# Performance work log

Hardware: AMD Instinct MI355X
Metric: run time of the kernel (lower is better)

The kernel has to match this reference:

```python
import jax, jax.numpy as jnp
import numpy as np

NUM_HEADS = 16


def dct_matrix(n, dtype=jnp.float32):
    # Orthonormal DCT-II matrix, matching the torch double-loop construction.
    i = jnp.arange(n, dtype=dtype)[:, None]
    j = jnp.arange(n, dtype=dtype)[None, :]
    m = jnp.sqrt(2.0 / n) * jnp.cos(jnp.pi * i * (2.0 * j + 1.0) / (2.0 * n))
    m = m.at[0, :].set(jnp.sqrt(1.0 / n))
    return m


def setup_inputs() -> dict:
    key = jax.random.key(0)
    ks = jax.random.split(key, 7)
    B, N, C = 8, 1024, 1024
    n_tasks, n_frq = 10, 3000
    return {
        "x": jax.random.normal(ks[0], (B, N, C), jnp.float32),
        "W_qkv": jax.random.normal(ks[1], (3 * C, C), jnp.float32) * 0.02,
        "W_proj": jax.random.normal(ks[2], (C, C), jnp.float32) * 0.02,
        "b_proj": jnp.zeros((C,), jnp.float32),
        "coef_k": jax.random.normal(ks[3], (n_tasks, n_frq), jnp.float32),
        "coef_v": jax.random.normal(ks[4], (n_tasks, n_frq), jnp.float32),
        "indices": jax.random.randint(ks[5], (n_tasks, n_frq), 0, C * C, jnp.int32),
        "task": 4,
    }


def _dct_lora_weight(coef, idx, Bm, d, dtype):
    # Scatter per-task frequency coefficients into the d x d DCT plane and sum
    # across tasks (sum commutes with the linear inverse transform), then
    # inverse 2D DCT: W = Bm^T @ S @ Bm.
    S = jnp.zeros((d * d,), dtype).at[idx.reshape(-1)].add(coef.reshape(-1))
    return Bm.T @ S.reshape(d, d) @ Bm


def reference(x, W_qkv, W_proj, b_proj, coef_k, coef_v, indices, task):
    B, N, C = x.shape
    H = NUM_HEADS
    hd = C // H
    scale = hd ** (-0.5)

    qkv = (x @ W_qkv.T).reshape(B, N, 3, H, hd).transpose(2, 0, 3, 1, 4)
    q, k, v = qkv[0], qkv[1], qkv[2]  # each (B, H, N, hd)

    T = task + 1  # tasks 0..task participate
    Bm = dct_matrix(C, x.dtype)
    Wk = _dct_lora_weight(coef_k[:T], indices[:T], Bm, C, x.dtype)
    Wv = _dct_lora_weight(coef_v[:T], indices[:T], Bm, C, x.dtype)

    # F.linear(x, W) == x @ W.T ; reshape to heads as in torch code
    k = k + (x @ Wk.T).reshape(B, N, H, hd).transpose(0, 2, 1, 3)
    v = v + (x @ Wv.T).reshape(B, N, H, hd).transpose(0, 2, 1, 3)

    attn = jax.nn.softmax(jnp.einsum("bhnd,bhmd->bhnm", q, k) * scale, axis=-1)
    out = jnp.einsum("bhnm,bhmd->bhnd", attn, v)
    out = out.transpose(0, 2, 1, 3).reshape(B, N, C)
    return out @ W_proj.T + b_proj
```

## Files before the change

kernel.cpp:

```cpp
#include <hip/hip_runtime.h>
#include <math.h>

#define NFRQ 3000

typedef __bf16 bf16;
typedef __attribute__((ext_vector_type(8))) __bf16 bf16x8;
typedef __attribute__((ext_vector_type(4))) __bf16 bf16x4;
typedef __attribute__((ext_vector_type(4))) float floatx4;

__device__ __forceinline__ floatx4 mfma16(bf16x8 a, bf16x8 b, floatx4 c) {
  return __builtin_amdgcn_mfma_f32_16x16x32_bf16(a, b, c, 0, 0, 0);
}

__device__ __forceinline__ void async_load16(const bf16* g, bf16* l) {
  __builtin_amdgcn_global_load_lds(
      (const __attribute__((address_space(1))) unsigned int*)g,
      (__attribute__((address_space(3))) unsigned int*)l, 16, 0, 0);
}

__device__ __forceinline__ float fexp2(float x) {
  return __builtin_amdgcn_exp2f(x);
}

__global__ __launch_bounds__(256) void prep_kernel(
    const float* __restrict__ W_qkv, const float* __restrict__ W_proj,
    const float* __restrict__ x, const float* __restrict__ Sf,
    bf16* __restrict__ Bmtb, bf16* __restrict__ Wcbq,
    bf16* __restrict__ Wprojb, bf16* __restrict__ xb,
    bf16* __restrict__ S2b) {
  int r = blockIdx.x;
  if (r < 1024) {
    int base = r * 1024 + (int)threadIdx.x * 4;
    const float cst = 0.04419417382415922f;
    const float w = 1.5339807878856412e-3f;
    bf16x4 o;
#pragma unroll
    for (int u = 0; u < 4; ++u) {
      int t = base + u;
      int j = t >> 10, i = t & 1023;
      int K = (i * (2 * j + 1)) & 4095;
      float v = (i == 0) ? 0.03125f : cst * __cosf((float)K * w);
      o[u] = (__bf16)v;
    }
    *(bf16x4*)&Bmtb[base] = o;
    return;
  }
  const float* src;
  bf16* dst;
  float scale = 1.0f;
  int i;
  if (r < 2048) {
    i = (r - 1024) * 256 + threadIdx.x;
    src = W_qkv; dst = Wcbq;
    scale = 0.18033688011112042f;
  } else if (r < 3072) {
    i = (r - 2048) * 256 + threadIdx.x;
    src = W_proj; dst = Wprojb;
  } else if (r < 11264) {
    i = (r - 3072) * 256 + threadIdx.x;
    src = x; dst = xb;
  } else {
    i = (r - 11264) * 256 + threadIdx.x;
    src = Sf; dst = S2b;
  }
  float4 f = ((const float4*)src)[i];
  bf16x4 o = {(__bf16)(f.x * scale), (__bf16)(f.y * scale),
              (__bf16)(f.z * scale), (__bf16)(f.w * scale)};
  *(bf16x4*)&dst[(size_t)i * 4] = o;
}

__global__ __launch_bounds__(256) void scatter_s(const float* __restrict__ coef_k,
                                                 const float* __restrict__ coef_v,
                                                 const int* __restrict__ idx,
                                                 const int* __restrict__ task,
                                                 float* __restrict__ S) {
  int nz = blockIdx.x * 256 + threadIdx.x;
  if (nz >= 10 * NFRQ || nz >= (*task + 1) * NFRQ) return;
  int id = idx[nz];
  atomicAdd(S + id, coef_k[nz]);
  atomicAdd(S + (1u << 20) + id, coef_v[nz]);
}

__global__ __launch_bounds__(512, 2) void gemm256_qkv(const bf16* __restrict__ A,
                                                      const bf16* __restrict__ B,
                                                      bf16* __restrict__ Cb,
                                                      bf16* __restrict__ vt) {
  __shared__ bf16 As[2][256][64];
  __shared__ bf16 Bs[2][256][64];
  int t = threadIdx.x, w = t >> 6, lane = t & 63;
  int q15 = lane & 15, quad = lane >> 4;
  int lid = blockIdx.x + gridDim.x * blockIdx.y;
  int band = gridDim.y >> 3;
  int xcd = lid & 7, tt = lid >> 3;
  int by = xcd * band + tt % band;
  int bx = tt / band;
  int m0 = by * 256, n0 = bx * 256;
  int wm = (w >> 2) * 128, wn = (w & 3) * 64;

  floatx4 acc[8][4];
#pragma unroll
  for (int i = 0; i < 8; ++i)
#pragma unroll
    for (int j = 0; j < 4; ++j) acc[i][j] = (floatx4){0.f, 0.f, 0.f, 0.f};

  int sr = lane >> 3, sc = lane & 7;
  const bf16* Agl = A + (size_t)(m0 + sr) * 1024 + (sc ^ sr) * 8;
  const bf16* Bgl = B + (size_t)(n0 + sr) * 1024 + (sc ^ sr) * 8;

#pragma unroll
  for (int s = 0; s < 4; ++s) {
    int rb = w * 32 + s * 8;
    async_load16(Agl + (size_t)rb * 1024, &As[0][rb][0]);
    async_load16(Bgl + (size_t)rb * 1024, &Bs[0][rb][0]);
  }

  for (int kt = 0; kt < 16; ++kt) {
    int cur = kt & 1;
    if (kt + 1 < 16) {
      int k0 = (kt + 1) * 64;
#pragma unroll
      for (int s = 0; s < 4; ++s) {
        int rb = w * 32 + s * 8;
        async_load16(Agl + (size_t)rb * 1024 + k0, &As[cur ^ 1][rb][0]);
        async_load16(Bgl + (size_t)rb * 1024 + k0, &Bs[cur ^ 1][rb][0]);
      }
      asm volatile("s_waitcnt vmcnt(8)\n\ts_barrier" ::: "memory");
    } else {
      asm volatile("s_waitcnt vmcnt(0)\n\ts_barrier" ::: "memory");
    }
    int rp = q15 & 7;
#pragma unroll
    for (int kk = 0; kk < 2; ++kk) {
      int kc = kk * 4 + quad;
      int ksw = (kc ^ rp) * 8;
      bf16x8 af[8], bfr[4];
#pragma unroll
      for (int i = 0; i < 8; ++i)
        af[i] = *(const bf16x8*)&As[cur][wm + i * 16 + q15][ksw];
#pragma unroll
      for (int j = 0; j < 4; ++j)
        bfr[j] = *(const bf16x8*)&Bs[cur][wn + j * 16 + q15][ksw];
#pragma unroll
      for (int i = 0; i < 8; ++i)
#pragma unroll
        for (int j = 0; j < 4; ++j)
          acc[i][j] = mfma16(af[i], bfr[j], acc[i][j]);
    }
    asm volatile("s_waitcnt lgkmcnt(0)\n\ts_barrier" ::: "memory");
  }

  if (n0 >= 2048) {
#pragma unroll
    for (int i = 0; i < 8; ++i) {
      int gm = m0 + wm + i * 16 + quad * 4;
      int p = gm >> 10, mi = gm & 1023;
#pragma unroll
      for (int j = 0; j < 4; ++j) {
        int vchan = (n0 + wn - 2048) + j * 16 + q15;
        bf16x4 pk = {(__bf16)acc[i][j][0], (__bf16)acc[i][j][1],
                     (__bf16)acc[i][j][2], (__bf16)acc[i][j][3]};
        *(bf16x4*)&vt[((((size_t)p << 10) | vchan) << 10) | mi] = pk;
      }
    }
    return;
  }

#pragma unroll
  for (int i = 0; i < 8; ++i)
#pragma unroll
    for (int r = 0; r < 4; ++r) {
      int gm = m0 + wm + i * 16 + quad * 4 + r;
      size_t rowo = (size_t)gm * 3072 + n0 + wn;
#pragma unroll
      for (int j = 0; j < 4; ++j) {
        int col = j * 16 + q15;
        Cb[rowo + col] = (__bf16)acc[i][j][r];
      }
    }
}

__global__ __launch_bounds__(512) void gemm256_proj(const bf16* __restrict__ A,
                                                    const bf16* __restrict__ B,
                                                    float* __restrict__ Cf,
                                                    const float* __restrict__ bias) {
  __shared__ bf16 As[2][256][64];
  __shared__ bf16 Bs[2][128][64];
  int t = threadIdx.x, w = t >> 6, lane = t & 63;
  int q15 = lane & 15, quad = lane >> 4;
  int lid = blockIdx.x + gridDim.x * blockIdx.y;
  int band = gridDim.y >> 3;
  int xcd = lid & 7, tt = lid >> 3;
  int by = xcd * band + tt % band;
  int bx = tt / band;
  int m0 = by * 256, n0 = bx * 128;
  int wm = (w >> 2) * 128, wn = (w & 3) * 32;

  floatx4 acc[8][2];
#pragma unroll
  for (int i = 0; i < 8; ++i)
#pragma unroll
    for (int j = 0; j < 2; ++j) acc[i][j] = (floatx4){0.f, 0.f, 0.f, 0.f};

  int sr = lane >> 3, sc = lane & 7;
  const bf16* Agl = A + (size_t)(m0 + sr) * 1024 + (sc ^ sr) * 8;
  const bf16* Bgl = B + (size_t)(n0 + sr) * 1024 + (sc ^ sr) * 8;

#pragma unroll
  for (int s = 0; s < 4; ++s)
    async_load16(Agl + (size_t)(w * 32 + s * 8) * 1024, &As[0][w * 32 + s * 8][0]);
#pragma unroll
  for (int s = 0; s < 2; ++s)
    async_load16(Bgl + (size_t)(w * 16 + s * 8) * 1024, &Bs[0][w * 16 + s * 8][0]);

  for (int kt = 0; kt < 16; ++kt) {
    int cur = kt & 1;
    if (kt + 1 < 16) {
      int k0 = (kt + 1) * 64;
#pragma unroll
      for (int s = 0; s < 4; ++s)
        async_load16(Agl + (size_t)(w * 32 + s * 8) * 1024 + k0,
                     &As[cur ^ 1][w * 32 + s * 8][0]);
#pragma unroll
      for (int s = 0; s < 2; ++s)
        async_load16(Bgl + (size_t)(w * 16 + s * 8) * 1024 + k0,
                     &Bs[cur ^ 1][w * 16 + s * 8][0]);
      asm volatile("s_waitcnt vmcnt(6)\n\ts_barrier" ::: "memory");
    } else {
      asm volatile("s_waitcnt vmcnt(0)\n\ts_barrier" ::: "memory");
    }
    int rp = q15 & 7;
#pragma unroll
    for (int kk = 0; kk < 2; ++kk) {
      int kc = kk * 4 + quad;
      int ksw = (kc ^ rp) * 8;
      bf16x8 af[8], bfr[2];
#pragma unroll
      for (int i = 0; i < 8; ++i)
        af[i] = *(const bf16x8*)&As[cur][wm + i * 16 + q15][ksw];
#pragma unroll
      for (int j = 0; j < 2; ++j)
        bfr[j] = *(const bf16x8*)&Bs[cur][wn + j * 16 + q15][ksw];
#pragma unroll
      for (int i = 0; i < 8; ++i)
#pragma unroll
        for (int j = 0; j < 2; ++j)
          acc[i][j] = mfma16(af[i], bfr[j], acc[i][j]);
    }
    asm volatile("s_waitcnt lgkmcnt(0)\n\ts_barrier" ::: "memory");
  }

#pragma unroll
  for (int i = 0; i < 8; ++i)
#pragma unroll
    for (int r = 0; r < 4; ++r) {
      int gm = m0 + wm + i * 16 + quad * 4 + r;
      size_t rowo = (size_t)gm * 1024 + n0 + wn;
#pragma unroll
      for (int j = 0; j < 2; ++j) {
        int col = j * 16 + q15;
        Cf[rowo + col] = acc[i][j][r] + bias[n0 + wn + col];
      }
    }
}

__global__ __launch_bounds__(256) void gemm64_bf16_nt(const bf16* __restrict__ A,
                                                      const bf16* __restrict__ B,
                                                      bf16* __restrict__ Cb,
                                                      float* __restrict__ Cf,
                                                      const float* __restrict__ addend,
                                                      const float* __restrict__ bias,
                                                      bf16* __restrict__ vt,
                                                      int vt_col0,
                                                      int N) {
  __shared__ bf16 As[2][4][64][8];
  __shared__ bf16 Bs[2][4][64][8];
  size_t zoff = (size_t)blockIdx.z << 20;
  B += zoff;
  if (Cb) Cb += zoff;
  if (addend) addend += zoff;
  int t = threadIdx.x, w = t >> 6, lane = t & 63;
  int q15 = lane & 15, quad = lane >> 4;
  int lid = blockIdx.x + gridDim.x * blockIdx.y;
  int band = gridDim.y >> 3;
  int xcd = lid & 7, tt = lid >> 3;
  int by = xcd * band + tt % band;
  int bx = tt / band;
  int m0 = by * 64, n0 = bx * 64;
  int wm = (w >> 1) * 32, wn = (w & 1) * 32;
  floatx4 acc[2][2];
#pragma unroll
  for (int i = 0; i < 2; ++i)
#pragma unroll
    for (int j = 0; j < 2; ++j) acc[i][j] = (floatx4){0.f, 0.f, 0.f, 0.f};

  const bf16* Ag = A + (size_t)(m0 + lane) * 1024 + w * 8;
  const bf16* Bg = B + (size_t)(n0 + lane) * 1024 + w * 8;

  async_load16(Ag, &As[0][w][0][0]);
  async_load16(Bg, &Bs[0][w][0][0]);

  for (int it = 0; it < 32; ++it) {
    int cur = it & 1;
    __syncthreads();
    if (it + 1 < 32) {
      int k0 = (it + 1) * 32;
      async_load16(Ag + k0, &As[cur ^ 1][w][0][0]);
      async_load16(Bg + k0, &Bs[cur ^ 1][w][0][0]);
    }
    bf16x8 af[2], bfr[2];
#pragma unroll
    for (int i = 0; i < 2; ++i)
      af[i] = *(const bf16x8*)&As[cur][quad][wm + i * 16 + q15][0];
#pragma unroll
    for (int j = 0; j < 2; ++j)
      bfr[j] = *(const bf16x8*)&Bs[cur][quad][wn + j * 16 + q15][0];
#pragma unroll
    for (int i = 0; i < 2; ++i)
#pragma unroll
      for (int j = 0; j < 2; ++j) acc[i][j] = mfma16(af[i], bfr[j], acc[i][j]);
  }

  if (vt && (n0 + wn) >= vt_col0) {
#pragma unroll
    for (int i = 0; i < 2; ++i) {
      int gm = m0 + wm + i * 16 + quad * 4;
      int p = gm >> 10, mi = gm & 1023;
#pragma unroll
      for (int j = 0; j < 2; ++j) {
        int vchan = (n0 + wn - vt_col0) + j * 16 + q15;
        bf16x4 pk = {(__bf16)acc[i][j][0], (__bf16)acc[i][j][1],
                     (__bf16)acc[i][j][2], (__bf16)acc[i][j][3]};
        *(bf16x4*)&vt[((((size_t)p << 10) | vchan) << 10) | mi] = pk;
      }
    }
    return;
  }

#pragma unroll
  for (int i = 0; i < 2; ++i)
#pragma unroll
    for (int r = 0; r < 4; ++r) {
      int gm = m0 + wm + i * 16 + quad * 4 + r;
      size_t rowo = (size_t)gm * N + n0 + wn;
#pragma unroll
      for (int j = 0; j < 2; ++j) {
        int col = j * 16 + q15;
        float v = acc[i][j][r];
        if (Cf) {
          Cf[rowo + col] = v + (bias ? bias[n0 + wn + col] : 0.f);
        } else {
          if (addend) v += addend[rowo + col];
          Cb[rowo + col] = (__bf16)v;
        }
      }
    }
}

__global__ __launch_bounds__(256) void attn_mfma(const bf16* __restrict__ qkvb,
                                                 const bf16* __restrict__ Vt,
                                                 bf16* __restrict__ attn_out) {
  __shared__ __align__(16) char smem[40960];
  bf16 (*Qs)[128][8] = (bf16(*)[128][8])smem;
  bf16* PsB = (bf16*)smem;
  bf16 (*Ks)[8][64][8] = (bf16(*)[8][64][8])(smem + 16384);
  bf16 (*Vs)[64][8] = (bf16(*)[64][8])(smem + 32768);

  int t = threadIdx.x, w = t >> 6, lane = t & 63;
  int q15 = lane & 15, quad = lane >> 4;
  int lid = blockIdx.x + (blockIdx.y << 3);
  int xcd = lid & 7, rr = lid >> 3;
  int q0 = (rr & 7) * 128;
  int bh = xcd + ((rr >> 3) << 3);
  int b = bh >> 4, h = bh & 15;

  const bf16* Qg = qkvb + (size_t)(b * 1024 + q0) * 3072 + h * 64;
  const bf16* Kg = qkvb + (size_t)(b * 1024) * 3072 + 1024 + h * 64;
  const bf16* Vg = Vt + (size_t)(bh * 64) * 1024;

#pragma unroll
  for (int cc = 0; cc < 2; ++cc) {
    int kc = w * 2 + cc;
    async_load16(Qg + (size_t)lane * 3072 + kc * 8,        &Qs[kc][0][0]);
    async_load16(Qg + (size_t)(64 + lane) * 3072 + kc * 8, &Qs[kc][64][0]);
  }
  {
    const bf16* Kg2 = Kg + (size_t)lane * 3072;
    const bf16* Vg2 = Vg + (size_t)lane * 1024;
    async_load16(Kg2 + (w * 2) * 8,     &Ks[0][w * 2][0][0]);
    async_load16(Kg2 + (w * 2 + 1) * 8, &Ks[0][w * 2 + 1][0][0]);
    async_load16(Vg2 + (w * 2) * 8,     &Vs[w * 2][0][0]);
    async_load16(Vg2 + (w * 2 + 1) * 8, &Vs[w * 2 + 1][0][0]);
  }
  __syncthreads();

  bf16x8 qfr[2][2];
#pragma unroll
  for (int ks = 0; ks < 2; ++ks)
#pragma unroll
    for (int nt = 0; nt < 2; ++nt)
      qfr[ks][nt] = *(const bf16x8*)&Qs[ks * 4 + quad][w * 32 + nt * 16 + q15][0];

  floatx4 oacc[4][2];
  float l_i[2] = {0.f, 0.f};
#pragma unroll
  for (int nt = 0; nt < 2; ++nt)
#pragma unroll
    for (int mt = 0; mt < 4; ++mt) oacc[mt][nt] = (floatx4){0.f, 0.f, 0.f, 0.f};

  for (int kt = 0; kt < 16; ++kt) {
    int cur = kt & 1;
    asm volatile("s_waitcnt vmcnt(2) lgkmcnt(0)\n\ts_barrier" ::: "memory");
    if (kt + 1 < 16) {
      int kv0n = (kt + 1) * 64;
      const bf16* Kg3 = Kg + (size_t)(kv0n + lane) * 3072;
      async_load16(Kg3 + (w * 2) * 8,     &Ks[cur ^ 1][w * 2][0][0]);
      async_load16(Kg3 + (w * 2 + 1) * 8, &Ks[cur ^ 1][w * 2 + 1][0][0]);
    }

    floatx4 sacc[4][2];
#pragma unroll
    for (int mt = 0; mt < 4; ++mt)
#pragma unroll
      for (int nt = 0; nt < 2; ++nt) sacc[mt][nt] = (floatx4){0.f, 0.f, 0.f, 0.f};
#pragma unroll
    for (int ks = 0; ks < 2; ++ks) {
      bf16x8 kf[4];
#pragma unroll
      for (int mt = 0; mt < 4; ++mt)
        kf[mt] = *(const bf16x8*)&Ks[cur][ks * 4 + quad][mt * 16 + q15][0];
#pragma unroll
      for (int mt = 0; mt < 4; ++mt)
#pragma unroll
        for (int nt = 0; nt < 2; ++nt)
          sacc[mt][nt] = mfma16(kf[mt], qfr[ks][nt], sacc[mt][nt]);
    }

#pragma unroll
    for (int nt = 0; nt < 2; ++nt) {
      float rsum = 0.f;
#pragma unroll
      for (int mt = 0; mt < 4; ++mt)
#pragma unroll
        for (int r = 0; r < 4; ++r) {
          float p = fexp2(sacc[mt][nt][r]);
          sacc[mt][nt][r] = p;
          rsum += p;
        }
      rsum += __shfl_xor(rsum, 16);
      rsum += __shfl_xor(rsum, 32);
      l_i[nt] += rsum;
    }

#pragma unroll
    for (int nt = 0; nt < 2; ++nt)
#pragma unroll
      for (int mt = 0; mt < 4; ++mt) {
        bf16x4 pk = {(__bf16)sacc[mt][nt][0], (__bf16)sacc[mt][nt][1],
                     (__bf16)sacc[mt][nt][2], (__bf16)sacc[mt][nt][3]};
        int kc = mt * 2 + (quad >> 1);
        *(bf16x4*)&PsB[(size_t)(w * 2 + nt) * 1024 + kc * 128 + q15 * 8 + (quad & 1) * 4] = pk;
      }

    if (kt + 1 < 16)
      asm volatile("s_waitcnt vmcnt(2)\n\ts_barrier" ::: "memory");
    else
      asm volatile("s_waitcnt vmcnt(0)\n\ts_barrier" ::: "memory");

#pragma unroll
    for (int ks = 0; ks < 2; ++ks) {
      bf16x8 vf[4], pf[2];
#pragma unroll
      for (int mt = 0; mt < 4; ++mt)
        vf[mt] = *(const bf16x8*)&Vs[ks * 4 + quad][mt * 16 + q15][0];
#pragma unroll
      for (int nt = 0; nt < 2; ++nt)
        pf[nt] = *(const bf16x8*)&PsB[(size_t)(w * 2 + nt) * 1024 + (ks * 4 + quad) * 128 + q15 * 8];
#pragma unroll
      for (int mt = 0; mt < 4; ++mt)
#pragma unroll
        for (int nt = 0; nt < 2; ++nt) oacc[mt][nt] = mfma16(vf[mt], pf[nt], oacc[mt][nt]);
    }

    if (kt + 1 < 16) {
      asm volatile("s_waitcnt lgkmcnt(0)\n\ts_barrier" ::: "memory");
      int kv0n = (kt + 1) * 64;
      const bf16* Vg3 = Vg + (size_t)lane * 1024 + kv0n;
      async_load16(Vg3 + (w * 2) * 8,     &Vs[w * 2][0][0]);
      async_load16(Vg3 + (w * 2 + 1) * 8, &Vs[w * 2 + 1][0][0]);
    }
  }

  __syncthreads();
  bf16* T = (bf16*)smem + w * 2304;
#pragma unroll
  for (int nt = 0; nt < 2; ++nt) {
    float inv = 1.f / l_i[nt];
#pragma unroll
    for (int mt = 0; mt < 4; ++mt) {
      bf16x4 pk = {(__bf16)(oacc[mt][nt][0] * inv), (__bf16)(oacc[mt][nt][1] * inv),
                   (__bf16)(oacc[mt][nt][2] * inv), (__bf16)(oacc[mt][nt][3] * inv)};
      *(bf16x4*)&T[(nt * 16 + q15) * 72 + mt * 16 + quad * 4] = pk;
    }
  }
  __syncthreads();
  int row = lane >> 1, ch = (lane & 1) * 32;
  const bf16* Tr = T + row * 72 + ch;
  bf16* outp = attn_out + (size_t)(b * 1024 + q0 + w * 32 + row) * 1024 + h * 64 + ch;
#pragma unroll
  for (int i = 0; i < 4; ++i) *(bf16x8*)&outp[i * 8] = *(const bf16x8*)&Tr[i * 8];
}

extern "C" void kernel_launch(void* const* d_in, const int* in_sizes, int n_in,
                              void* d_out, int out_size, void* d_ws, size_t ws_size,
                              hipStream_t stream) {
  (void)in_sizes; (void)n_in; (void)out_size; (void)ws_size;
  const float* x       = (const float*)d_in[0];
  const float* W_qkv   = (const float*)d_in[1];
  const float* W_proj  = (const float*)d_in[2];
  const float* b_proj  = (const float*)d_in[3];
  const float* coef_k  = (const float*)d_in[4];
  const float* coef_v  = (const float*)d_in[5];
  const int*   indices = (const int*)d_in[6];
  const int*   task    = (const int*)d_in[7];

  char* w8 = (char*)d_ws;
  float* Sf     = (float*)(w8);
  bf16*  S2b    = (bf16*) (w8 + (8u  << 20));
  bf16*  Tt     = (bf16*) (w8 + (12u << 20));
  bf16*  Bmtb   = (bf16*) (w8 + (16u << 20));
  bf16*  Wcb    = (bf16*) (w8 + (18u << 20));
  bf16*  xb     = (bf16*) (w8 + (24u << 20));
  bf16*  qkvb   = (bf16*) (w8 + (40u << 20));
  bf16*  Vt     = (bf16*) (w8 + (88u << 20));
  bf16*  Wprojb = (bf16*) (w8 + (104u << 20));
  bf16*  attnout= (bf16*) (w8);

  hipMemsetAsync(Sf, 0, (size_t)8 << 20, stream);
  scatter_s<<<118, 256, 0, stream>>>(coef_k, coef_v, indices, task, Sf);
  prep_kernel<<<13312, 256, 0, stream>>>(W_qkv, W_proj, x, Sf,
                                         Bmtb, Wcb, Wprojb, xb, S2b);

  gemm64_bf16_nt<<<dim3(16, 32), 256, 0, stream>>>(S2b, Bmtb, nullptr, nullptr,
                                                   nullptr, nullptr, Tt, 0, 1024);
  gemm64_bf16_nt<<<dim3(16, 16, 2), 256, 0, stream>>>(Bmtb, Tt, Wcb + (1u << 20), nullptr,
                                                      W_qkv + (1u << 20), nullptr, nullptr,
                                                      1 << 30, 1024);

  gemm256_qkv<<<dim3(12, 32), 512, 0, stream>>>(xb, Wcb, qkvb, Vt);

  attn_mfma<<<dim3(8, 128), 256, 0, stream>>>(qkvb, Vt, attnout);

  gemm256_proj<<<dim3(8, 32), 512, 0, stream>>>(attnout, Wprojb, (float*)d_out, b_proj);
}
```

Measured before the change: 304.3 us.

## Double attention query tile to 256 rows per block for K/V reuse

Each attention block now handles 256 query rows instead of 128, with each wave processing two 32-row query sub-tiles against the same K and V tiles staged in shared memory. This halves the K/V global-to-LDS traffic and the per-block loop overhead, and the grid shrinks from 1024 to 512 blocks. The cost is more LDS per block (56 KB), double the accumulator registers, and fewer blocks, which may lower occupancy and latency hiding.

Result: no change. 307.9 us (+1.2%).

```diff
diff --git a/kernel.cpp b/kernel.cpp
--- a/kernel.cpp
+++ b/kernel.cpp
@@ -359,18 +359,18 @@
 __global__ __launch_bounds__(256) void attn_mfma(const bf16* __restrict__ qkvb,
                                                  const bf16* __restrict__ Vt,
                                                  bf16* __restrict__ attn_out) {
-  __shared__ __align__(16) char smem[40960];
-  bf16 (*Qs)[128][8] = (bf16(*)[128][8])smem;
+  __shared__ __align__(16) char smem[57344];
+  bf16 (*Qs)[256][8] = (bf16(*)[256][8])smem;
   bf16* PsB = (bf16*)smem;
-  bf16 (*Ks)[8][64][8] = (bf16(*)[8][64][8])(smem + 16384);
-  bf16 (*Vs)[64][8] = (bf16(*)[64][8])(smem + 32768);
+  bf16 (*Ks)[8][64][8] = (bf16(*)[8][64][8])(smem + 32768);
+  bf16 (*Vs)[64][8] = (bf16(*)[64][8])(smem + 49152);
 
   int t = threadIdx.x, w = t >> 6, lane = t & 63;
   int q15 = lane & 15, quad = lane >> 4;
   int lid = blockIdx.x + (blockIdx.y << 3);
   int xcd = lid & 7, rr = lid >> 3;
-  int q0 = (rr & 7) * 128;
-  int bh = xcd + ((rr >> 3) << 3);
+  int q0 = (rr & 3) * 256;
+  int bh = xcd + ((rr >> 2) << 3);
   int b = bh >> 4, h = bh & 15;
 
   const bf16* Qg = qkvb + (size_t)(b * 1024 + q0) * 3072 + h * 64;
@@ -380,8 +380,9 @@
 #pragma unroll
   for (int cc = 0; cc < 2; ++cc) {
     int kc = w * 2 + cc;
-    async_load16(Qg + (size_t)lane * 3072 + kc * 8,        &Qs[kc][0][0]);
-    async_load16(Qg + (size_t)(64 + lane) * 3072 + kc * 8, &Qs[kc][64][0]);
+#pragma unroll
+    for (int rb = 0; rb < 4; ++rb)
+      async_load16(Qg + (size_t)(rb * 64 + lane) * 3072 + kc * 8, &Qs[kc][rb * 64][0]);
   }
   {
     const bf16* Kg2 = Kg + (size_t)lane * 3072;
@@ -393,19 +394,24 @@
   }
   __syncthreads();
 
-  bf16x8 qfr[2][2];
-#pragma unroll
-  for (int ks = 0; ks < 2; ++ks)
+  bf16x8 qfr[2][2][2];
+#pragma unroll
+  for (int qt = 0; qt < 2; ++qt)
+#pragma unroll
+    for (int ks = 0; ks < 2; ++ks)
+#pragma unroll
+      for (int nt = 0; nt < 2; ++nt)
+        qfr[qt][ks][nt] =
+            *(const bf16x8*)&Qs[ks * 4 + quad][qt * 128 + w * 32 + nt * 16 + q15][0];
+
+  floatx4 oacc[2][4][2];
+  float l_i[2][2] = {{0.f, 0.f}, {0.f, 0.f}};
+#pragma unroll
+  for (int qt = 0; qt < 2; ++qt)
 #pragma unroll
     for (int nt = 0; nt < 2; ++nt)
-      qfr[ks][nt] = *(const bf16x8*)&Qs[ks * 4 + quad][w * 32 + nt * 16 + q15][0];
-
-  floatx4 oacc[4][2];
-  float l_i[2] = {0.f, 0.f};
-#pragma unroll
-  for (int nt = 0; nt < 2; ++nt)
-#pragma unroll
-    for (int mt = 0; mt < 4; ++mt) oacc[mt][nt] = (floatx4){0.f, 0.f, 0.f, 0.f};
+#pragma unroll
+      for (int mt = 0; mt < 4; ++mt) oacc[qt][mt][nt] = (floatx4){0.f, 0.f, 0.f, 0.f};
 
   for (int kt = 0; kt < 16; ++kt) {
     int cur = kt & 1;
@@ -417,49 +423,50 @@
       async_load16(Kg3 + (w * 2 + 1) * 8, &Ks[cur ^ 1][w * 2 + 1][0][0]);
     }
 
-    floatx4 sacc[4][2];
-#pragma unroll
-    for (int mt = 0; mt < 4; ++mt)
-#pragma unroll
-      for (int nt = 0; nt < 2; ++nt) sacc[mt][nt] = (floatx4){0.f, 0.f, 0.f, 0.f};
-#pragma unroll
-    for (int ks = 0; ks < 2; ++ks) {
-      bf16x8 kf[4];
+#pragma unroll
+    for (int qt = 0; qt < 2; ++qt) {
+      floatx4 sacc[4][2];
 #pragma unroll
       for (int mt = 0; mt < 4; ++mt)
-        kf[mt] = *(const bf16x8*)&Ks[cur][ks * 4 + quad][mt * 16 + q15][0];
-#pragma unroll
-      for (int mt = 0; mt < 4; ++mt)
-#pragma unroll
-        for (int nt = 0; nt < 2; ++nt)
-          sacc[mt][nt] = mfma16(kf[mt], qfr[ks][nt], sacc[mt][nt]);
-    }
-
-#pragma unroll
-    for (int nt = 0; nt < 2; ++nt) {
-      float rsum = 0.f;
-#pragma unroll
-      for (int mt = 0; mt < 4; ++mt)
-#pragma unroll
-        for (int r = 0; r < 4; ++r) {
-          float p = fexp2(sacc[mt][nt][r]);
-          sacc[mt][nt][r] = p;
-          rsum += p;
+#pragma unroll
+        for (int nt = 0; nt < 2; ++nt) sacc[mt][nt] = (floatx4){0.f, 0.f, 0.f, 0.f};
+#pragma unroll
+      for (int ks = 0; ks < 2; ++ks) {
+        bf16x8 kf[4];
+#pragma unroll
+        for (int mt = 0; mt < 4; ++mt)
+          kf[mt] = *(const bf16x8*)&Ks[cur][ks * 4 + quad][mt * 16 + q15][0];
+#pragma unroll
+        for (int mt = 0; mt < 4; ++mt)
+#pragma unroll
+          for (int nt = 0; nt < 2; ++nt)
+            sacc[mt][nt] = mfma16(kf[mt], qfr[qt][ks][nt], sacc[mt][nt]);
+      }
+#pragma unroll
+      for (int nt = 0; nt < 2; ++nt) {
+        float rsum = 0.f;
+#pragma unroll
+        for (int mt = 0; mt < 4; ++mt)
+#pragma unroll
+          for (int r = 0; r < 4; ++r) {
+            float p = fexp2(sacc[mt][nt][r]);
+            sacc[mt][nt][r] = p;
+            rsum += p;
+          }
+        rsum += __shfl_xor(rsum, 16);
+        rsum += __shfl_xor(rsum, 32);
+        l_i[qt][nt] += rsum;
+      }
+#pragma unroll
+      for (int nt = 0; nt < 2; ++nt)
+#pragma unroll
+        for (int mt = 0; mt < 4; ++mt) {
+          bf16x4 pk = {(__bf16)sacc[mt][nt][0], (__bf16)sacc[mt][nt][1],
+                       (__bf16)sacc[mt][nt][2], (__bf16)sacc[mt][nt][3]};
+          int kc = mt * 2 + (quad >> 1);
+          *(bf16x4*)&PsB[(size_t)(w * 4 + qt * 2 + nt) * 1024 + kc * 128 + q15 * 8 + (quad & 1) * 4] = pk;
         }
-      rsum += __shfl_xor(rsum, 16);
-      rsum += __shfl_xor(rsum, 32);
-      l_i[nt] += rsum;
-    }
-
-#pragma unroll
-    for (int nt = 0; nt < 2; ++nt)
-#pragma unroll
-      for (int mt = 0; mt < 4; ++mt) {
-        bf16x4 pk = {(__bf16)sacc[mt][nt][0], (__bf16)sacc[mt][nt][1],
-                     (__bf16)sacc[mt][nt][2], (__bf16)sacc[mt][nt][3]};
-        int kc = mt * 2 + (quad >> 1);
-        *(bf16x4*)&PsB[(size_t)(w * 2 + nt) * 1024 + kc * 128 + q15 * 8 + (quad & 1) * 4] = pk;
-      }
+    }
 
     if (kt + 1 < 16)
       asm volatile("s_waitcnt vmcnt(2)\n\ts_barrier" ::: "memory");
@@ -468,17 +475,22 @@
 
 #pragma unroll
     for (int ks = 0; ks < 2; ++ks) {
-      bf16x8 vf[4], pf[2];
+      bf16x8 vf[4];
 #pragma unroll
       for (int mt = 0; mt < 4; ++mt)
         vf[mt] = *(const bf16x8*)&Vs[ks * 4 + quad][mt * 16 + q15][0];
 #pragma unroll
-      for (int nt = 0; nt < 2; ++nt)
-        pf[nt] = *(const bf16x8*)&PsB[(size_t)(w * 2 + nt) * 1024 + (ks * 4 + quad) * 128 + q15 * 8];
-#pragma unroll
-      for (int mt = 0; mt < 4; ++mt)
-#pragma unroll
-        for (int nt = 0; nt < 2; ++nt) oacc[mt][nt] = mfma16(vf[mt], pf[nt], oacc[mt][nt]);
+      for (int qt = 0; qt < 2; ++qt) {
+        bf16x8 pf[2];
+#pragma unroll
+        for (int nt = 0; nt < 2; ++nt)
+          pf[nt] = *(const bf16x8*)&PsB[(size_t)(w * 4 + qt * 2 + nt) * 1024 + (ks * 4 + quad) * 128 + q15 * 8];
+#pragma unroll
+        for (int mt = 0; mt < 4; ++mt)
+#pragma unroll
+          for (int nt = 0; nt < 2; ++nt)
+            oacc[qt][mt][nt] = mfma16(vf[mt], pf[nt], oacc[qt][mt][nt]);
+      }
     }
 
     if (kt + 1 < 16) {
@@ -490,24 +502,27 @@
     }
   }
 
-  __syncthreads();
   bf16* T = (bf16*)smem + w * 2304;
 #pragma unroll
-  for (int nt = 0; nt < 2; ++nt) {
-    float inv = 1.f / l_i[nt];
-#pragma unroll
-    for (int mt = 0; mt < 4; ++mt) {
-      bf16x4 pk = {(__bf16)(oacc[mt][nt][0] * inv), (__bf16)(oacc[mt][nt][1] * inv),
-                   (__bf16)(oacc[mt][nt][2] * inv), (__bf16)(oacc[mt][nt][3] * inv)};
-      *(bf16x4*)&T[(nt * 16 + q15) * 72 + mt * 16 + quad * 4] = pk;
-    }
-  }
-  __syncthreads();
-  int row = lane >> 1, ch = (lane & 1) * 32;
-  const bf16* Tr = T + row * 72 + ch;
-  bf16* outp = attn_out + (size_t)(b * 1024 + q0 + w * 32 + row) * 1024 + h * 64 + ch;
-#pragma unroll
-  for (int i = 0; i < 4; ++i) *(bf16x8*)&outp[i * 8] = *(const bf16x8*)&Tr[i * 8];
+  for (int qt = 0; qt < 2; ++qt) {
+    __syncthreads();
+#pragma unroll
+    for (int nt = 0; nt < 2; ++nt) {
+      float inv = 1.f / l_i[qt][nt];
+#pragma unroll
+      for (int mt = 0; mt < 4; ++mt) {
+        bf16x4 pk = {(__bf16)(oacc[qt][mt][nt][0] * inv), (__bf16)(oacc[qt][mt][nt][1] * inv),
+                     (__bf16)(oacc[qt][mt][nt][2] * inv), (__bf16)(oacc[qt][mt][nt][3] * inv)};
+        *(bf16x4*)&T[(nt * 16 + q15) * 72 + mt * 16 + quad * 4] = pk;
+      }
+    }
+    __syncthreads();
+    int row = lane >> 1, ch = (lane & 1) * 32;
+    const bf16* Tr = T + row * 72 + ch;
+    bf16* outp = attn_out + (size_t)(b * 1024 + q0 + qt * 128 + w * 32 + row) * 1024 + h * 64 + ch;
+#pragma unroll
+    for (int i = 0; i < 4; ++i) *(bf16x8*)&outp[i * 8] = *(const bf16x8*)&Tr[i * 8];
+  }
 }
 
 extern "C" void kernel_launch(void* const* d_in, const int* in_sizes, int n_in,
@@ -548,7 +563,7 @@
 
   gemm256_qkv<<<dim3(12, 32), 512, 0, stream>>>(xb, Wcb, qkvb, Vt);
 
-  attn_mfma<<<dim3(8, 128), 256, 0, stream>>>(qkvb, Vt, attnout);
+  attn_mfma<<<dim3(8, 64), 256, 0, stream>>>(qkvb, Vt, attnout);
 
   gemm256_proj<<<dim3(8, 32), 512, 0, stream>>>(attnout, Wprojb, (float*)d_out, b_proj);
 }
```
